# Optimization experiments

Hardware: AMD Instinct MI355X
Metric: run time of the kernel (lower is better)

The kernel has to match this reference:

```python
import jax, jax.numpy as jnp
import numpy as np

_NORM12 = np.array([[3,1,1,1,3,3,3,3],[1,3,1,1,3,3,3,3],[1,1,3,1,3,3,3,3],[1,1,1,3,3,3,3,3],[3,3,3,1,3,3,1,1],[3,3,3,1,3,1,3,1],[3,3,3,1,1,3,3,1],[3,3,3,1,3,1,1,3],[3,3,3,1,1,3,1,3],[3,3,3,1,1,1,3,3],[3,3,1,3,3,3,1,1],[3,3,1,3,3,1,3,1],[3,3,1,3,1,3,3,1],[3,3,1,3,3,1,1,3],[3,3,1,3,1,3,1,3],[3,3,1,3,1,1,3,3],[3,1,3,3,3,3,1,1],[3,1,3,3,3,1,3,1],[3,1,3,3,1,3,3,1],[3,1,3,3,3,1,1,3],[3,1,3,3,1,3,1,3],[1,3,3,3,1,1,3,3],[1,3,3,3,3,3,1,1],[1,3,3,3,3,1,3,1],[1,3,3,3,1,3,3,1],[1,3,3,3,3,1,1,3],[1,3,3,3,1,3,1,3],[1,1,3,3,1,3,3,3],[3,3,1,1,3,3,3,1]], dtype=np.float32) / 2.0


def _build_tables():
    # abs_grid: nonneg half-integer D8+1/2 abs patterns with norm^2 <= 10 (227 rows,
    # lexicographically sorted like torch.unique(dim=0)), plus 29 norm-12 extras -> 256 rows.
    vals = np.arange(4, dtype=np.float32) + 0.5  # {0.5,1.5,2.5,3.5}
    mesh = np.stack(np.meshgrid(*([vals] * 8), indexing='ij'), axis=-1).reshape(-1, 8)
    d8abs = mesh[(mesh ** 2).sum(-1) <= 10.0]
    d8abs = np.unique(d8abs, axis=0)
    abs_grid = np.concatenate([d8abs, _NORM12], axis=0)  # [256, 8]
    grid_abs_odd = (np.round(abs_grid.sum(-1)).astype(np.int64) % 2) == 1
    # grid_part = E8 lattice points (even # of sign flips of abs rows, last coord
    # pre-negated for odd-sum rows) filtered to: at most one of the first 7 coords < 0
    # and min(first 7) >= -0.5. This equals _E8P_GRID[_PARITY_IDX] + 0.25 after filtering.
    ap = abs_grid.copy()
    ap[:, 7] *= np.where(grid_abs_odd, -1.0, 1.0).astype(np.float32)
    bits = (np.arange(256)[:, None] >> np.arange(8)[None, :]) & 1
    signs = (1.0 - 2.0 * bits[(bits.sum(-1) % 2) == 0]).astype(np.float32)  # [128, 8]
    pts = (ap[:, None, :] * signs[None, :, :]).reshape(-1, 8)
    keep = ((pts[:, :7] < 0).sum(-1) <= 1) & (pts[:, :7].min(-1) >= -0.5)
    grid_part = pts[keep]
    grid_part_norm = (grid_part ** 2).sum(-1)
    # part_abs_map: nearest abs_grid row of |grid_part| (exact match; same argmax form as torch)
    scores = 2.0 * np.abs(grid_part) @ abs_grid.T - (abs_grid ** 2).sum(-1)
    part_abs_map = scores.argmax(-1).astype(np.int32)
    return grid_part, grid_part_norm, part_abs_map, grid_abs_odd


def setup_inputs() -> dict:
    gp, gpn, pam, gao = _build_tables()
    key = jax.random.key(0)
    X = jax.random.normal(key, (131072, 8), dtype=jnp.float32)
    return {
        'X': X,
        'grid_part': jnp.asarray(gp, dtype=jnp.float32),
        'grid_part_norm': jnp.asarray(gpn, dtype=jnp.float32),
        'part_abs_map': jnp.asarray(pam, dtype=jnp.int32),
        'grid_abs_odd': jnp.asarray(gao),
        'bit_map': jnp.asarray(2 ** np.arange(8), dtype=jnp.int32),
    }


_PERM = jnp.array([0, 2, 4, 6, 1, 3, 5, 7])


def _fast_quantize_part(X, grid_part, grid_part_norm, part_abs_map, grid_abs_odd, bit_map, parity):
    Xa = jnp.abs(X)
    neg = X < 0
    odd_row = (neg.sum(-1) % 2) == 1                       # [m]
    flip = (jnp.arange(8) == 7)[None, :] & odd_row[:, None]  # negate col 7 for odd rows
    X_part = jnp.where(flip, -Xa, Xa)
    mask = 1.0 - 2.0 * neg.astype(X.dtype)
    mask = jnp.where(flip, -mask, mask)
    scores = 2.0 * (X_part @ grid_part.T) - grid_part_norm  # [m, G]
    Xqidx = jnp.argmax(scores, axis=-1)
    roundout = grid_part[Xqidx]                            # [m, 8]
    vals = roundout * mask
    err = jnp.sqrt(jnp.sum((X - vals) ** 2, axis=-1))
    abs_idx = part_abs_map[Xqidx].astype(jnp.int32)
    sign_mask = ((roundout < 0) ^ (mask < 0))[:, _PERM]
    sign_mask = sign_mask.at[:, 7].set(sign_mask[:, 7] ^ grid_abs_odd[abs_idx])
    sign_mask = sign_mask.at[:, 0].set(sign_mask[:, 0] ^ parity)
    mask_idx = jnp.sum(sign_mask.astype(jnp.int32) * bit_map, axis=-1)
    idx = (abs_idx << 8) + mask_idx
    return vals, idx, err


def reference(X, grid_part, grid_part_norm, part_abs_map, grid_abs_odd, bit_map):
    quarter = jnp.asarray(0.25, X.dtype)
    pv, pi, pe = _fast_quantize_part(X + quarter, grid_part, grid_part_norm, part_abs_map, grid_abs_odd, bit_map, True)
    mv, mi, me = _fast_quantize_part(X - quarter, grid_part, grid_part_norm, part_abs_map, grid_abs_odd, bit_map, False)
    which = pe < me
    final_vals = jnp.where(which[:, None], pv - quarter, mv + quarter)
    final_idx = jnp.where(which, pi, mi)
    return final_vals, final_idx
```

## Files before the change

kernel.cpp:

```cpp
#include <hip/hip_runtime.h>
#include <math.h>

#define NT   256
#define ROWS 128
#define NW   4
#define MAXA 320

static __device__ __forceinline__ unsigned f16_ru(float v) {
    _Float16 h = (_Float16)v;
    unsigned short b;
    __builtin_memcpy(&b, &h, 2);
    if ((float)h < v) b = (b & 0x8000) ? (unsigned short)(b - 1) : (unsigned short)(b + 1);
    return (unsigned)b;
}
static __device__ __forceinline__ float f16_lo(unsigned bits) {
    unsigned short s = (unsigned short)(bits & 0xffffu);
    _Float16 h;
    __builtin_memcpy(&h, &s, 2);
    return (float)h;
}

__global__ __launch_bounds__(NT, 4)
void e8p_quant_kernel(const float* __restrict__ X,
                      const float* __restrict__ gp,
                      const float* __restrict__ gn,
                      const int* __restrict__ pam,
                      float* __restrict__ out,
                      int N, int G)
{
#pragma clang fp contract(off)
    __shared__ float4         labsA[MAXA];
    __shared__ float4         labsB[MAXA];
    __shared__ unsigned short lmeta[MAXA];
    __shared__ float    cb_bb[2][NW][ROWS];
    __shared__ float    cb_ev[2][NW][ROWS];
    __shared__ unsigned cb_h [2][NW][ROWS];
    __shared__ unsigned cb_ij[2][NW][ROWS];

    const int NG = pam[G - 1] + 1;

    const float4* gp4 = reinterpret_cast<const float4*>(gp);
    for (int j = threadIdx.x; j < G; j += NT) {
        int a = pam[j];
        bool st = (j == 0) || (pam[j - 1] != a);
        if (st) {
            float4 A = gp4[2 * j], B = gp4[2 * j + 1];
            labsA[a] = A;
            labsB[a] = B;
            float gv[8] = {A.x, A.y, A.z, A.w, B.x, B.y, B.z, B.w};
            int hm = 0;
#pragma unroll
            for (int k = 0; k < 7; ++k) hm |= int(fabsf(gv[k]) == 0.5f) << k;
            int nc = (int)((gn[j] - 2.0f) * 4.0f + 0.5f);
            lmeta[a] = (unsigned short)(hm | (nc << 8));
        }
    }
    __syncthreads();

    const int lane = threadIdx.x & 63;
    const int w    = threadIdx.x >> 6;
    const int rb   = blockIdx.x * ROWS;

    float xf[2][8], xp[2][8], xm[2][8];
    int msbp[2], msbm[2], oddp[2], oddm[2];
    float DLT[2];
    const float4* x4 = reinterpret_cast<const float4*>(X);
#pragma unroll
    for (int rr = 0; rr < 2; ++rr) {
        int r = rb + lane + (rr << 6);
        int rc = (r < N) ? r : (N - 1);
        float4 a0 = x4[2 * rc], a1 = x4[2 * rc + 1];
        float xr[8] = {a0.x, a0.y, a0.z, a0.w, a1.x, a1.y, a1.z, a1.w};
        int nbp = 0, nbm = 0; float Sp = 0.f, Sm = 0.f;
#pragma unroll
        for (int k = 0; k < 8; ++k) {
            xf[rr][k] = xr[k];
            float sp = xr[k] + 0.25f, sm = xr[k] - 0.25f;
            nbp |= int(sp < 0.f) << k;  nbm |= int(sm < 0.f) << k;
            xp[rr][k] = fabsf(sp);  xm[rr][k] = fabsf(sm);
            Sp += xp[rr][k]; Sm += xm[rr][k];
        }
        int op = __popc(nbp) & 1, om = __popc(nbm) & 1;
        if (op) xp[rr][7] = -xp[rr][7];
        if (om) xm[rr][7] = -xm[rr][7];
        oddp[rr] = op; oddm[rr] = om;
        msbp[rr] = nbp ^ (op << 7);  msbm[rr] = nbm ^ (om << 7);
        DLT[rr] = fmaf(3.5f * fmaxf(Sp, Sm), 3.0e-6f, 2.5e-5f);
    }

    float bt[2][2], ev[2][2], s0v[2][2], s1v[2][2];
    int   i0[2][2], i1[2][2];
#pragma unroll
    for (int rr = 0; rr < 2; ++rr)
#pragma unroll
        for (int pp = 0; pp < 2; ++pp) {
            bt[rr][pp] = -3.0e38f; ev[rr][pp] = -3.0e38f;
            s0v[rr][pp] = -3.0e38f; s1v[rr][pp] = -3.0e38f;
            i0[rr][pp] = 0; i1[rr][pp] = 0;
        }

    const int Q = (NG + NW - 1) / NW;
    const int abeg = w * Q, aend = min(NG, abeg + Q);

#pragma unroll 2
    for (int a = abeg; a < aend; ++a) {
        float4 ga = labsA[a], gb = labsB[a];
        int meta = __builtin_amdgcn_readfirstlane((int)lmeta[a]);
        int hm = meta & 0x7f;
        float nnh = fmaf(-0.125f, (float)(meta >> 8), -1.0f);
        float g0 = ga.x, g1 = ga.y, g2 = ga.z, g3 = ga.w;
        float g4 = gb.x, g5 = gb.y, g6 = gb.z, g7 = gb.w;
        float m2c7 = -2.0f * g7;

        float sc[2][2], wv[2][2], rm[2][2];
#pragma unroll
        for (int rr = 0; rr < 2; ++rr) {
            float s = fmaf(xp[rr][0], g0, nnh);
            s = fmaf(xp[rr][1], g1, s); s = fmaf(xp[rr][2], g2, s);
            s = fmaf(xp[rr][3], g3, s); s = fmaf(xp[rr][4], g4, s);
            s = fmaf(xp[rr][5], g5, s); s = fmaf(xp[rr][6], g6, s);
            s = fmaf(xp[rr][7], g7, s);
            sc[rr][0] = s;
            float t = fmaf(xm[rr][0], g0, nnh);
            t = fmaf(xm[rr][1], g1, t); t = fmaf(xm[rr][2], g2, t);
            t = fmaf(xm[rr][3], g3, t); t = fmaf(xm[rr][4], g4, t);
            t = fmaf(xm[rr][5], g5, t); t = fmaf(xm[rr][6], g6, t);
            t = fmaf(xm[rr][7], g7, t);
            sc[rr][1] = t;
            wv[rr][0] = fmaf(m2c7, xp[rr][7], s);
            wv[rr][1] = fmaf(m2c7, xm[rr][7], t);
            rm[rr][0] = s; rm[rr][1] = t;
        }
#pragma unroll
        for (int i = 0; i < 7; ++i) {
            if (hm & (1 << i)) {
                rm[0][0] = fmaxf(rm[0][0], wv[0][0] - xp[0][i]);
                rm[0][1] = fmaxf(rm[0][1], wv[0][1] - xm[0][i]);
                rm[1][0] = fmaxf(rm[1][0], wv[1][0] - xp[1][i]);
                rm[1][1] = fmaxf(rm[1][1], wv[1][1] - xm[1][i]);
            }
        }
#pragma unroll
        for (int rr = 0; rr < 2; ++rr)
#pragma unroll
            for (int pp = 0; pp < 2; ++pp) {
                float v = rm[rr][pp];
                if (v >= bt[rr][pp]) {
                    ev[rr][pp] = fmaxf(ev[rr][pp], s1v[rr][pp]);
                    s1v[rr][pp] = s0v[rr][pp]; i1[rr][pp] = i0[rr][pp];
                    s0v[rr][pp] = v;           i0[rr][pp] = a;
                    bt[rr][pp] = fmaxf(bt[rr][pp], v - DLT[rr]);
                }
            }
    }

#pragma unroll
    for (int rr = 0; rr < 2; ++rr) {
        int rowL = lane + (rr << 6);
#pragma unroll
        for (int pp = 0; pp < 2; ++pp) {
            cb_bb[pp][w][rowL] = fmaxf(s0v[rr][pp], fmaxf(s1v[rr][pp], ev[rr][pp]));
            cb_ev[pp][w][rowL] = ev[rr][pp];
            cb_h [pp][w][rowL] = f16_ru(s0v[rr][pp]) | (f16_ru(s1v[rr][pp]) << 16);
            cb_ij[pp][w][rowL] = (unsigned)i0[rr][pp] | ((unsigned)i1[rr][pp] << 16);
        }
    }
    __syncthreads();

    const int t = threadIdx.x;
    if (t >= ROWS) return;
    const int row = rb + t;
    if (row >= N) return;
    const int rs = (t >= 64) ? 1 : 0;

    double xpd[8], xmd[8];
#pragma unroll
    for (int k = 0; k < 8; ++k) {
        double xd = (double)xf[rs][k];
        xpd[k] = fabs(xd + 0.25);
        xmd[k] = fabs(xd - 0.25);
    }
    if (oddp[rs]) xpd[7] = -xpd[7];
    if (oddm[rs]) xmd[7] = -xmd[7];

    auto evalRow = [&](int a, const double* xd, double& bd, int& brow, int& bflip) {
        float4 ga = labsA[a], gb = labsB[a];
        int meta = (int)lmeta[a];
        int hm = meta & 0x7f;
        double nd = 2.0 + 0.25 * (double)(meta >> 8);
        double a0=(double)ga.x, a1=(double)ga.y, a2=(double)ga.z, a3=(double)ga.w;
        double a4=(double)gb.x, a5=(double)gb.y, a6=(double)gb.z, a7=(double)gb.w;
        double s = xd[0] * a0;
        s = fma(xd[1], a1, s); s = fma(xd[2], a2, s); s = fma(xd[3], a3, s);
        s = fma(xd[4], a4, s); s = fma(xd[5], a5, s); s = fma(xd[6], a6, s);
        s = fma(xd[7], a7, s);
        double sc0 = fma(2.0, s, -nd);
        if (sc0 > bd) { bd = sc0; brow = a; bflip = -1; }
        double sb2 = sc0 - 4.0 * (xd[7] * a7);
#pragma unroll
        for (int i = 0; i < 7; ++i) {
            if (hm & (1 << i)) {
                double sv = sb2 - 2.0 * xd[i];
                if (sv > bd) { bd = sv; brow = a; bflip = i; }
            }
        }
    };

    auto resolve = [&](int pp, const double* xd, int& browO, int& bflipO) {
        float B = fmaxf(fmaxf(cb_bb[pp][0][t], cb_bb[pp][1][t]),
                        fmaxf(cb_bb[pp][2][t], cb_bb[pp][3][t]));
        float thr = B - DLT[rs];
        bool ok = (cb_ev[pp][0][t] < thr) && (cb_ev[pp][1][t] < thr) &&
                  (cb_ev[pp][2][t] < thr) && (cb_ev[pp][3][t] < thr);
        double bd = -1.0e300; int brow = 0, bflip = -1;
        if (ok) {
#pragma unroll
            for (int w2 = 0; w2 < NW; ++w2) {
                unsigned hh = cb_h[pp][w2][t], ij = cb_ij[pp][w2][t];
                if (f16_lo(hh >> 16) >= thr) evalRow((int)(ij >> 16), xd, bd, brow, bflip);
                if (f16_lo(hh & 0xffffu) >= thr) evalRow((int)(ij & 0xffffu), xd, bd, brow, bflip);
            }
        } else {
            for (int a = 0; a < NG; ++a) evalRow(a, xd, bd, brow, bflip);
        }
        browO = brow; bflipO = bflip;
    };

    int prow, pflip, mrow, mflip;
    resolve(0, xpd, prow, pflip);
    resolve(1, xmd, mrow, mflip);

    double vp[8], vm[8];
    double errP, errM; int idxP, idxM;
    auto finish = [&](int brow, int bflip, double sgn_quarter, int msb, int par,
                      double* v, double& errO, int& idxO) {
#pragma clang fp contract(off)
        float4 ga = labsA[brow], gb = labsB[brow];
        float g[8] = {ga.x, ga.y, ga.z, ga.w, gb.x, gb.y, gb.z, gb.w};
        if (bflip >= 0) {
#pragma unroll
            for (int k = 0; k < 7; ++k) if (bflip == k) g[k] = -g[k];
            g[7] = -g[7];
        }
        int gneg = 0; float sumabs = 0.0f;
#pragma unroll
        for (int k = 0; k < 8; ++k) {
            gneg |= int(g[k] < 0.0f) << k;
            sumabs += fabsf(g[k]);
        }
        double vv[8];
#pragma unroll
        for (int k = 0; k < 8; ++k) {
            unsigned u = __float_as_uint(g[k]) ^ ((((unsigned)msb >> k) & 1u) << 31);
            double val = (double)__uint_as_float(u);
            vv[k] = val;
            v[k] = val;
        }
        double d[8];
#pragma unroll
        for (int k = 0; k < 8; ++k) {
            double xs = (double)xf[rs][k] + sgn_quarter;
            d[k] = xs - vv[k];
        }
        double q0 = d[0]*d[0], q1 = d[1]*d[1], q2 = d[2]*d[2], q3 = d[3]*d[3];
        double q4 = d[4]*d[4], q5 = d[5]*d[5], q6 = d[6]*d[6], q7 = d[7]*d[7];
        double e = ((q0 + q1) + (q2 + q3)) + ((q4 + q5) + (q6 + q7));
        errO = sqrt(e);
        int godd = ((int)(sumabs + 0.5f)) & 1;
        int sb = gneg ^ msb;
        int mi = (((sb >> 0) & 1) ^ par)
               | (((sb >> 2) & 1) << 1)
               | (((sb >> 4) & 1) << 2)
               | (((sb >> 6) & 1) << 3)
               | (((sb >> 1) & 1) << 4)
               | (((sb >> 3) & 1) << 5)
               | (((sb >> 5) & 1) << 6)
               | ((((sb >> 7) & 1) ^ godd) << 7);
        idxO = (brow << 8) + mi;
    };

    finish(prow, pflip, +0.25, msbp[rs], 1, vp, errP, idxP);
    finish(mrow, mflip, -0.25, msbm[rs], 0, vm, errM, idxM);
    bool which = errP < errM;

    float ov[8];
#pragma unroll
    for (int k = 0; k < 8; ++k) {
        double o = which ? (vp[k] - 0.25) : (vm[k] + 0.25);
        ov[k] = (float)o;
    }
    float4* o4 = reinterpret_cast<float4*>(out + (size_t)row * 8);
    o4[0] = make_float4(ov[0], ov[1], ov[2], ov[3]);
    o4[1] = make_float4(ov[4], ov[5], ov[6], ov[7]);
    out[(size_t)N * 8 + row] = (float)(which ? idxP : idxM);
}

extern "C" void kernel_launch(void* const* d_in, const int* in_sizes, int n_in,
                              void* d_out, int out_size, void* d_ws, size_t ws_size,
                              hipStream_t stream)
{
    const float* X   = (const float*)d_in[0];
    const float* gp  = (const float*)d_in[1];
    const float* gn  = (const float*)d_in[2];
    const int*   pam = (const int*)d_in[3];
    float* out = (float*)d_out;

    int N = in_sizes[0] / 8;
    int G = in_sizes[1] / 8;
    int blocks = (N + ROWS - 1) / ROWS;
    e8p_quant_kernel<<<blocks, NT, 0, stream>>>(X, gp, gn, pam, out, N, G);
}
```

Before: 71.11 us.

## Process four rows per lane and use all threads in resolve phase

```diff
diff --git a/kernel.cpp b/kernel.cpp
--- a/kernel.cpp
+++ b/kernel.cpp
@@ -2,7 +2,8 @@
 #include <math.h>
 
 #define NT   256
-#define ROWS 128
+#define ROWS 256
+#define RPL  4
 #define NW   4
 #define MAXA 320
 
@@ -20,7 +21,7 @@
     return (float)h;
 }
 
-__global__ __launch_bounds__(NT, 4)
+__global__ __launch_bounds__(NT, 2)
 void e8p_quant_kernel(const float* __restrict__ X,
                       const float* __restrict__ gp,
                       const float* __restrict__ gn,
@@ -32,6 +33,9 @@
     __shared__ float4         labsA[MAXA];
     __shared__ float4         labsB[MAXA];
     __shared__ unsigned short lmeta[MAXA];
+    __shared__ float          xfs[ROWS][8];
+    __shared__ unsigned       lmsb[ROWS];
+    __shared__ float          ldlt[ROWS];
     __shared__ float    cb_bb[2][NW][ROWS];
     __shared__ float    cb_ev[2][NW][ROWS];
     __shared__ unsigned cb_h [2][NW][ROWS];
@@ -61,20 +65,20 @@
     const int w    = threadIdx.x >> 6;
     const int rb   = blockIdx.x * ROWS;
 
-    float xf[2][8], xp[2][8], xm[2][8];
-    int msbp[2], msbm[2], oddp[2], oddm[2];
-    float DLT[2];
+    float xp[RPL][8], xm[RPL][8];
+    float DLT[RPL];
     const float4* x4 = reinterpret_cast<const float4*>(X);
 #pragma unroll
-    for (int rr = 0; rr < 2; ++rr) {
-        int r = rb + lane + (rr << 6);
+    for (int rr = 0; rr < RPL; ++rr) {
+        int rowL = lane + (rr << 6);
+        int r = rb + rowL;
         int rc = (r < N) ? r : (N - 1);
         float4 a0 = x4[2 * rc], a1 = x4[2 * rc + 1];
         float xr[8] = {a0.x, a0.y, a0.z, a0.w, a1.x, a1.y, a1.z, a1.w};
         int nbp = 0, nbm = 0; float Sp = 0.f, Sm = 0.f;
 #pragma unroll
         for (int k = 0; k < 8; ++k) {
-            xf[rr][k] = xr[k];
+            xfs[rowL][k] = xr[k];
             float sp = xr[k] + 0.25f, sm = xr[k] - 0.25f;
             nbp |= int(sp < 0.f) << k;  nbm |= int(sm < 0.f) << k;
             xp[rr][k] = fabsf(sp);  xm[rr][k] = fabsf(sm);
@@ -83,15 +87,17 @@
         int op = __popc(nbp) & 1, om = __popc(nbm) & 1;
         if (op) xp[rr][7] = -xp[rr][7];
         if (om) xm[rr][7] = -xm[rr][7];
-        oddp[rr] = op; oddm[rr] = om;
-        msbp[rr] = nbp ^ (op << 7);  msbm[rr] = nbm ^ (om << 7);
+        int msbp = nbp ^ (op << 7), msbm = nbm ^ (om << 7);
+        if (w == 0) lmsb[rowL] = (unsigned)msbp | ((unsigned)msbm << 8)
+                               | ((unsigned)op << 16) | ((unsigned)om << 17);
         DLT[rr] = fmaf(3.5f * fmaxf(Sp, Sm), 3.0e-6f, 2.5e-5f);
-    }
-
-    float bt[2][2], ev[2][2], s0v[2][2], s1v[2][2];
-    int   i0[2][2], i1[2][2];
-#pragma unroll
-    for (int rr = 0; rr < 2; ++rr)
+        if (w == 0) ldlt[rowL] = DLT[rr];
+    }
+
+    float bt[RPL][2], ev[RPL][2], s0v[RPL][2], s1v[RPL][2];
+    int   i0[RPL][2], i1[RPL][2];
+#pragma unroll
+    for (int rr = 0; rr < RPL; ++rr)
 #pragma unroll
         for (int pp = 0; pp < 2; ++pp) {
             bt[rr][pp] = -3.0e38f; ev[rr][pp] = -3.0e38f;
@@ -112,21 +118,19 @@
         float g4 = gb.x, g5 = gb.y, g6 = gb.z, g7 = gb.w;
         float m2c7 = -2.0f * g7;
 
-        float sc[2][2], wv[2][2], rm[2][2];
-#pragma unroll
-        for (int rr = 0; rr < 2; ++rr) {
+        float wv[RPL][2], rm[RPL][2];
+#pragma unroll
+        for (int rr = 0; rr < RPL; ++rr) {
             float s = fmaf(xp[rr][0], g0, nnh);
             s = fmaf(xp[rr][1], g1, s); s = fmaf(xp[rr][2], g2, s);
             s = fmaf(xp[rr][3], g3, s); s = fmaf(xp[rr][4], g4, s);
             s = fmaf(xp[rr][5], g5, s); s = fmaf(xp[rr][6], g6, s);
             s = fmaf(xp[rr][7], g7, s);
-            sc[rr][0] = s;
             float t = fmaf(xm[rr][0], g0, nnh);
             t = fmaf(xm[rr][1], g1, t); t = fmaf(xm[rr][2], g2, t);
             t = fmaf(xm[rr][3], g3, t); t = fmaf(xm[rr][4], g4, t);
             t = fmaf(xm[rr][5], g5, t); t = fmaf(xm[rr][6], g6, t);
             t = fmaf(xm[rr][7], g7, t);
-            sc[rr][1] = t;
             wv[rr][0] = fmaf(m2c7, xp[rr][7], s);
             wv[rr][1] = fmaf(m2c7, xm[rr][7], t);
             rm[rr][0] = s; rm[rr][1] = t;
@@ -134,14 +138,15 @@
 #pragma unroll
         for (int i = 0; i < 7; ++i) {
             if (hm & (1 << i)) {
-                rm[0][0] = fmaxf(rm[0][0], wv[0][0] - xp[0][i]);
-                rm[0][1] = fmaxf(rm[0][1], wv[0][1] - xm[0][i]);
-                rm[1][0] = fmaxf(rm[1][0], wv[1][0] - xp[1][i]);
-                rm[1][1] = fmaxf(rm[1][1], wv[1][1] - xm[1][i]);
+#pragma unroll
+                for (int rr = 0; rr < RPL; ++rr) {
+                    rm[rr][0] = fmaxf(rm[rr][0], wv[rr][0] - xp[rr][i]);
+                    rm[rr][1] = fmaxf(rm[rr][1], wv[rr][1] - xm[rr][i]);
+                }
             }
         }
 #pragma unroll
-        for (int rr = 0; rr < 2; ++rr)
+        for (int rr = 0; rr < RPL; ++rr)
 #pragma unroll
             for (int pp = 0; pp < 2; ++pp) {
                 float v = rm[rr][pp];
@@ -155,7 +160,7 @@
     }
 
 #pragma unroll
-    for (int rr = 0; rr < 2; ++rr) {
+    for (int rr = 0; rr < RPL; ++rr) {
         int rowL = lane + (rr << 6);
 #pragma unroll
         for (int pp = 0; pp < 2; ++pp) {
@@ -168,20 +173,23 @@
     __syncthreads();
 
     const int t = threadIdx.x;
-    if (t >= ROWS) return;
     const int row = rb + t;
     if (row >= N) return;
-    const int rs = (t >= 64) ? 1 : 0;
+
+    unsigned mb = lmsb[t];
+    const int msbp = (int)(mb & 0xffu), msbm = (int)((mb >> 8) & 0xffu);
+    const int oddp = (int)((mb >> 16) & 1u), oddm = (int)((mb >> 17) & 1u);
+    const float DLTt = ldlt[t];
 
     double xpd[8], xmd[8];
 #pragma unroll
     for (int k = 0; k < 8; ++k) {
-        double xd = (double)xf[rs][k];
+        double xd = (double)xfs[t][k];
         xpd[k] = fabs(xd + 0.25);
         xmd[k] = fabs(xd - 0.25);
     }
-    if (oddp[rs]) xpd[7] = -xpd[7];
-    if (oddm[rs]) xmd[7] = -xmd[7];
+    if (oddp) xpd[7] = -xpd[7];
+    if (oddm) xmd[7] = -xmd[7];
 
     auto evalRow = [&](int a, const double* xd, double& bd, int& brow, int& bflip) {
         float4 ga = labsA[a], gb = labsB[a];
@@ -209,7 +217,7 @@
     auto resolve = [&](int pp, const double* xd, int& browO, int& bflipO) {
         float B = fmaxf(fmaxf(cb_bb[pp][0][t], cb_bb[pp][1][t]),
                         fmaxf(cb_bb[pp][2][t], cb_bb[pp][3][t]));
-        float thr = B - DLT[rs];
+        float thr = B - DLTt;
         bool ok = (cb_ev[pp][0][t] < thr) && (cb_ev[pp][1][t] < thr) &&
                   (cb_ev[pp][2][t] < thr) && (cb_ev[pp][3][t] < thr);
         double bd = -1.0e300; int brow = 0, bflip = -1;
@@ -259,7 +267,7 @@
         double d[8];
 #pragma unroll
         for (int k = 0; k < 8; ++k) {
-            double xs = (double)xf[rs][k] + sgn_quarter;
+            double xs = (double)xfs[t][k] + sgn_quarter;
             d[k] = xs - vv[k];
         }
         double q0 = d[0]*d[0], q1 = d[1]*d[1], q2 = d[2]*d[2], q3 = d[3]*d[3];
@@ -279,8 +287,8 @@
         idxO = (brow << 8) + mi;
     };
 
-    finish(prow, pflip, +0.25, msbp[rs], 1, vp, errP, idxP);
-    finish(mrow, mflip, -0.25, msbm[rs], 0, vm, errM, idxM);
+    finish(prow, pflip, +0.25, msbp, 1, vp, errP, idxP);
+    finish(mrow, mflip, -0.25, msbm, 0, vm, errM, idxM);
     bool which = errP < errM;
 
     float ov[8];
```

After: 77.08 us. +8.4%, slower.
